# Kernel optimization log

Hardware: AMD Instinct MI355X
Metric: run time of the kernel (lower is better)

## Reference

```python
import jax, jax.numpy as jnp
import numpy as np

EPS = 1e-5
B, C, H, W, K = 16, 512, 64, 64, 32


def setup_inputs() -> dict:
    key = jax.random.key(0)
    ks = jax.random.split(key, 6)
    std = 1.0 / float(np.sqrt(K * C))
    return {
        "x": jax.random.normal(ks[0], (B, C, H, W), jnp.float32),
        "conv_w": jax.random.normal(ks[1], (C, C), jnp.float32) * (1.0 / np.sqrt(C)),
        "bn2_g": jnp.ones((C,), jnp.float32),
        "bn2_b": jnp.zeros((C,), jnp.float32),
        "bn2_m": jnp.zeros((C,), jnp.float32),
        "bn2_v": jnp.ones((C,), jnp.float32),
        "codewords": jax.random.uniform(ks[2], (K, C), jnp.float32, -std, std),
        "scale": jax.random.uniform(ks[3], (K,), jnp.float32, -1.0, 0.0),
        "bn1_g": jnp.ones((K,), jnp.float32),
        "bn1_b": jnp.zeros((K,), jnp.float32),
        "bn1_m": jnp.zeros((K,), jnp.float32),
        "bn1_v": jnp.ones((K,), jnp.float32),
        "fc_w": jax.random.normal(ks[4], (C, C), jnp.float32) * (1.0 / np.sqrt(C)),
        "fc_b": jnp.zeros((C,), jnp.float32),
    }


def reference(x, conv_w, bn2_g, bn2_b, bn2_m, bn2_v, codewords, scale,
              bn1_g, bn1_b, bn1_m, bn1_v, fc_w, fc_b):
    b, c, h, w = x.shape
    k = codewords.shape[0]
    # encoding_project: 1x1 conv (no bias) + BatchNorm2d (inference) + ReLU
    proj = jnp.einsum('oc,bchw->bohw', conv_w, x)
    s2 = (jax.lax.rsqrt(bn2_v + EPS) * bn2_g)[None, :, None, None]
    proj = jax.nn.relu((proj - bn2_m[None, :, None, None]) * s2 + bn2_b[None, :, None, None])
    # Encoding: scaled-L2 softmax assignment + residual aggregation
    feats = proj.reshape(b, c, h * w).transpose(0, 2, 1)          # (B, N, C)
    x2 = jnp.sum(feats * feats, axis=-1)                          # (B, N)
    c2 = jnp.sum(codewords * codewords, axis=-1)                  # (K,)
    xc = jnp.einsum('bnc,kc->bnk', feats, codewords)              # (B, N, K)
    dist = scale[None, None, :] * (x2[..., None] - 2.0 * xc + c2[None, None, :])
    assign = jax.nn.softmax(dist, axis=2)                         # (B, N, K)
    # sum_n w[b,n,k] * (x[b,n,c] - c[k,c])  without materializing (B,N,K,C)
    encoded = (jnp.einsum('bnk,bnc->bkc', assign, feats)
               - jnp.einsum('bnk,kc->bkc', assign, codewords))    # (B, K, C)
    # BatchNorm1d over num_codes (inference) + ReLU
    s1 = (jax.lax.rsqrt(bn1_v + EPS) * bn1_g)[None, :, None]
    encoded = jax.nn.relu((encoded - bn1_m[None, :, None]) * s1 + bn1_b[None, :, None])
    encoding_feat = jnp.mean(encoded, axis=1)                     # (B, C)
    # fc -> sigmoid gate, residual relu
    gamma = jax.nn.sigmoid(encoding_feat @ fc_w.T + fc_b)         # (B, C)
    output = jax.nn.relu(x + x * gamma[:, :, None, None])
    return (encoding_feat, output)
```

## Files before the change

kernel.cpp:

```cpp
#include <hip/hip_runtime.h>
#include <hip/hip_bf16.h>

#define BB   16
#define CC   512
#define HWN  4096
#define KK   32
#define EPSF 1e-5f

typedef short bf16x8 __attribute__((ext_vector_type(8)));
typedef float f32x4  __attribute__((ext_vector_type(4)));

#define MFMA16 __builtin_amdgcn_mfma_f32_16x16x32_bf16

#define GLD16(g, l) __builtin_amdgcn_global_load_lds(                          \
    (const __attribute__((address_space(1))) void*)(g),                        \
    (__attribute__((address_space(3))) void*)(l), 16, 0, 0)

#define EADDR(o, n) ((o) * 136 + (((((n) >> 3) ^ (((o) >> 3) & 15))) << 3) + ((n) & 7))

static __device__ __forceinline__ unsigned short f2b(float f) {
    unsigned u = __builtin_bit_cast(unsigned, f);
    unsigned r = (u + 0x7FFFu + ((u >> 16) & 1u)) >> 16;
    return (unsigned short)r;
}

__global__ __launch_bounds__(256) void k_prep(const float* __restrict__ W,
                                              const float* __restrict__ cw,
                                              const float* __restrict__ scale,
                                              const float* __restrict__ g1,
                                              const float* __restrict__ b1,
                                              const float* __restrict__ m1,
                                              const float* __restrict__ v1,
                                              unsigned short* __restrict__ Wb,
                                              unsigned short* __restrict__ cwb,
                                              float* __restrict__ sc2,
                                              float* __restrict__ s1,
                                              float* __restrict__ t1) {
    int bid = blockIdx.x, t = threadIdx.x;
    if (bid < 256) {
        int i = (bid * 256 + t) * 4;
        float4 v = *(const float4*)(W + i);
        uint2 p;
        p.x = (unsigned)f2b(v.x) | ((unsigned)f2b(v.y) << 16);
        p.y = (unsigned)f2b(v.z) | ((unsigned)f2b(v.w) << 16);
        *(uint2*)(Wb + i) = p;
    } else if (bid < 272) {
        int i = ((bid - 256) * 256 + t) * 4;
        float4 v = *(const float4*)(cw + i);
        uint2 p;
        p.x = (unsigned)f2b(v.x) | ((unsigned)f2b(v.y) << 16);
        p.y = (unsigned)f2b(v.z) | ((unsigned)f2b(v.w) << 16);
        *(uint2*)(cwb + i) = p;
    } else {
        int k = t >> 3, l8 = t & 7;
        const float* row = cw + k * CC + l8 * 64;
        float s = 0.f;
#pragma unroll
        for (int i = 0; i < 16; i++) {
            float4 c4 = *(const float4*)(row + i * 4);
            s += c4.x * c4.x + c4.y * c4.y + c4.z * c4.z + c4.w * c4.w;
        }
        s += __shfl_xor(s, 1); s += __shfl_xor(s, 2); s += __shfl_xor(s, 4);
        if (l8 == 0) sc2[k] = scale[k] * s;
        if (t < KK) {
            float sv = rsqrtf(v1[t] + EPSF) * g1[t];
            s1[t] = sv;
            t1[t] = b1[t] - m1[t] * sv;
        }
    }
}

__global__ __launch_bounds__(256) void k_transpose(const float* __restrict__ x,
                                                   unsigned short* __restrict__ xT) {
    __shared__ float tile[64][65];
    int bid = blockIdx.x;
    int b   = bid >> 9;
    int rem = bid & 511;
    int c0  = (rem >> 6) * 64;
    int n0  = (rem & 63) * 64;
    int t = threadIdx.x;
#pragma unroll
    for (int p = 0; p < 4; p++) {
        int s = p * 256 + t;
        int row = s >> 4, col = (s & 15) * 4;
        float4 v = *(const float4*)(x + (size_t)(b * CC + c0 + row) * HWN + n0 + col);
        tile[row][col]     = v.x;
        tile[row][col + 1] = v.y;
        tile[row][col + 2] = v.z;
        tile[row][col + 3] = v.w;
    }
    __syncthreads();
    int nr = t >> 2;
    int cg = (t & 3) * 16;
    unsigned u[8];
#pragma unroll
    for (int j = 0; j < 8; j++) {
        u[j] = (unsigned)f2b(tile[cg + 2 * j][nr]) |
               ((unsigned)f2b(tile[cg + 2 * j + 1][nr]) << 16);
    }
    unsigned short* dst = xT + (size_t)(b * HWN + n0 + nr) * CC + c0 + cg;
    uint4 a; a.x = u[0]; a.y = u[1]; a.z = u[2]; a.w = u[3];
    uint4 c; c.x = u[4]; c.y = u[5]; c.z = u[6]; c.w = u[7];
    *(uint4*)(dst)     = a;
    *(uint4*)(dst + 8) = c;
}

__global__ __launch_bounds__(256) void k_conv_gemm(const unsigned short* __restrict__ xT,
                                                   const unsigned short* __restrict__ Wb,
                                                   const float* __restrict__ g2,
                                                   const float* __restrict__ b2,
                                                   const float* __restrict__ m2,
                                                   const float* __restrict__ v2,
                                                   unsigned short* __restrict__ feats,
                                                   unsigned short* __restrict__ featsT,
                                                   float* __restrict__ x2) {
    __shared__ __align__(16) short lds[17408];
    int bid = blockIdx.x;
    bid = (bid & 7) * 256 + (bid >> 3);
    int b   = bid >> 7;
    int rem = bid & 127;
    int m0  = (rem >> 2) * 128;
    int o0  = (rem & 3) * 128;
    int t = threadIdx.x, lane = t & 63, wave = t >> 6;
    int mb = (wave >> 1) * 64, ob = (wave & 1) * 64;
    int col_l = lane & 15, quad = lane >> 4;

    f32x4 zero = {0.f, 0.f, 0.f, 0.f};
    f32x4 acc[4][4];
#pragma unroll
    for (int i = 0; i < 4; i++)
#pragma unroll
        for (int j = 0; j < 4; j++) acc[i][j] = zero;

    const unsigned short* Abase = xT + (size_t)(b * HWN + m0) * CC;
    const unsigned short* Bbase = Wb + (size_t)o0 * CC;

#define CSTAGE(pp, bb) do {                                                   \
    int c0_ = (pp) * 32;                                                      \
    _Pragma("unroll")                                                         \
    for (int p2 = 0; p2 < 2; p2++) {                                          \
        int sbase = p2 * 256 + wave * 64;                                     \
        int s = sbase + lane;                                                 \
        int row = s >> 2, part = (s & 3) * 8;                                 \
        GLD16(Abase + (size_t)row * CC + c0_ + part,                          \
              (char*)lds + (bb) * 8192 + sbase * 16);                         \
        GLD16(Bbase + (size_t)row * CC + c0_ + part,                          \
              (char*)lds + 16384 + (bb) * 8192 + sbase * 16);                 \
    } } while (0)

#define CCOMP(bb) do {                                                        \
    bf16x8 af[4], bfv[4];                                                     \
    _Pragma("unroll")                                                         \
    for (int im = 0; im < 4; im++)                                            \
        af[im] = *(const bf16x8*)(&lds[(bb) * 4096 + (mb + im * 16 + col_l) * 32 + quad * 8]); \
    _Pragma("unroll")                                                         \
    for (int in = 0; in < 4; in++)                                            \
        bfv[in] = *(const bf16x8*)(&lds[8192 + (bb) * 4096 + (ob + in * 16 + col_l) * 32 + quad * 8]); \
    _Pragma("unroll")                                                         \
    for (int im = 0; im < 4; im++)                                            \
        _Pragma("unroll")                                                     \
        for (int in = 0; in < 4; in++)                                        \
            acc[im][in] = MFMA16(af[im], bfv[in], acc[im][in], 0, 0, 0);      \
    } while (0)

    CSTAGE(0, 0);
    for (int p = 0; p < 15; p++) {
        CSTAGE(p + 1, (p + 1) & 1);
        asm volatile("s_waitcnt vmcnt(4)" ::: "memory");
        __builtin_amdgcn_s_barrier();
        asm volatile("" ::: "memory");
        CCOMP(p & 1);
        asm volatile("s_waitcnt lgkmcnt(0)" ::: "memory");
        __builtin_amdgcn_s_barrier();
    }
    asm volatile("s_waitcnt vmcnt(0)" ::: "memory");
    __builtin_amdgcn_s_barrier();
    asm volatile("" ::: "memory");
    CCOMP(1);
    __syncthreads();

    float scv[4], offv[4];
#pragma unroll
    for (int in = 0; in < 4; in++) {
        int o = o0 + ob + in * 16 + col_l;
        float sv = rsqrtf(v2[o] + EPSF) * g2[o];
        scv[in]  = sv;
        offv[in] = b2[o] - m2[o] * sv;
    }
#pragma unroll
    for (int im = 0; im < 4; im++) {
        int n_l = mb + im * 16 + quad * 4;
        float vv[4][4];
#pragma unroll
        for (int in = 0; in < 4; in++)
#pragma unroll
            for (int r = 0; r < 4; r++)
                vv[in][r] = fmaxf(acc[im][in][r] * scv[in] + offv[in], 0.f);
#pragma unroll
        for (int in = 0; in < 4; in++) {
            int o_l = ob + in * 16 + col_l;
            uint2 pk;
            pk.x = (unsigned)f2b(vv[in][0]) | ((unsigned)f2b(vv[in][1]) << 16);
            pk.y = (unsigned)f2b(vv[in][2]) | ((unsigned)f2b(vv[in][3]) << 16);
            *(uint2*)(&lds[EADDR(o_l, n_l)]) = pk;
        }
#pragma unroll
        for (int r = 0; r < 4; r++) {
            float ss = vv[0][r] * vv[0][r] + vv[1][r] * vv[1][r] +
                       vv[2][r] * vv[2][r] + vv[3][r] * vv[3][r];
            ss += __shfl_xor(ss, 1); ss += __shfl_xor(ss, 2);
            ss += __shfl_xor(ss, 4); ss += __shfl_xor(ss, 8);
            if (col_l == 0) atomicAdd(&x2[b * HWN + m0 + n_l + r], ss);
        }
    }
    __syncthreads();

#pragma unroll
    for (int rr = 0; rr < 8; rr++) {
        int o = rr * 16 + (t >> 4);
        int n16 = t & 15;
        uint4 v = *(const uint4*)(&lds[EADDR(o, n16 * 8)]);
        *(uint4*)(featsT + (size_t)(b * CC + o0 + o) * HWN + m0 + n16 * 8) = v;
    }
#pragma unroll
    for (int rr = 0; rr < 8; rr++) {
        int n = rr * 16 + (t >> 4);
        int o16 = t & 15;
        unsigned u[4];
#pragma unroll
        for (int jj = 0; jj < 4; jj++) {
            unsigned short a = lds[EADDR(o16 * 8 + 2 * jj,     n)];
            unsigned short bsh = lds[EADDR(o16 * 8 + 2 * jj + 1, n)];
            u[jj] = (unsigned)a | ((unsigned)bsh << 16);
        }
        uint4 pk; pk.x = u[0]; pk.y = u[1]; pk.z = u[2]; pk.w = u[3];
        *(uint4*)(feats + (size_t)(b * HWN + m0 + n) * CC + o0 + o16 * 8) = pk;
    }
}

__global__ __launch_bounds__(256) void k_assign(const unsigned short* __restrict__ feats,
                                                const unsigned short* __restrict__ cwb,
                                                const float* __restrict__ x2,
                                                const float* __restrict__ scale,
                                                const float* __restrict__ sc2,
                                                unsigned short* __restrict__ assignT,
                                                float* __restrict__ asum) {
    __shared__ __align__(16) short lds2[24832];
    __shared__ float sl[KK], cl[KK];
    int bid = blockIdx.x;
    int b = bid >> 5, n0 = (bid & 31) * 128;
    int t = threadIdx.x, lane = t & 63, wave = t >> 6;
    int col_l = lane & 15, quad = lane >> 4;

#pragma unroll
    for (int p = 0; p < 8; p++) {
        int s = p * 256 + t;
        int row = s >> 6, c8 = (s & 63) * 8;
        *(uint4*)(&lds2[row * 520 + c8]) = *(const uint4*)(cwb + row * 512 + c8);
    }
    if (t < KK) { sl[t] = scale[t]; cl[t] = sc2[t]; }

    f32x4 zero = {0.f, 0.f, 0.f, 0.f};
    f32x4 acc[2][2];
    acc[0][0] = zero; acc[0][1] = zero; acc[1][0] = zero; acc[1][1] = zero;

    const unsigned short* Fbase = feats + (size_t)(b * HWN + n0) * CC;

#define ASTAGE(ci_, bb) do {                                                  \
    int c0_ = (ci_) * 32;                                                     \
    _Pragma("unroll")                                                         \
    for (int p2 = 0; p2 < 2; p2++) {                                          \
        int sbase = p2 * 256 + wave * 64;                                     \
        int s = sbase + lane;                                                 \
        GLD16(Fbase + (size_t)(s >> 2) * CC + c0_ + (s & 3) * 8,              \
              (char*)lds2 + 33280 + (bb) * 8192 + sbase * 16);                \
    } } while (0)

#define ACOMP(ci_, bb) do {                                                   \
    int c0_ = (ci_) * 32;                                                     \
    bf16x8 af0 = *(const bf16x8*)(&lds2[(col_l) * 520 + c0_ + quad * 8]);     \
    bf16x8 af1 = *(const bf16x8*)(&lds2[(16 + col_l) * 520 + c0_ + quad * 8]);\
    _Pragma("unroll")                                                         \
    for (int ct = 0; ct < 2; ct++) {                                          \
        bf16x8 bf = *(const bf16x8*)(&lds2[16640 + (bb) * 4096 +              \
                     (wave * 32 + ct * 16 + col_l) * 32 + quad * 8]);         \
        acc[0][ct] = MFMA16(af0, bf, acc[0][ct], 0, 0, 0);                    \
        acc[1][ct] = MFMA16(af1, bf, acc[1][ct], 0, 0, 0);                    \
    } } while (0)

    ASTAGE(0, 0);
    asm volatile("s_waitcnt lgkmcnt(0)" ::: "memory");
    for (int ci = 0; ci < 15; ci++) {
        ASTAGE(ci + 1, (ci + 1) & 1);
        asm volatile("s_waitcnt vmcnt(2)" ::: "memory");
        __builtin_amdgcn_s_barrier();
        asm volatile("" ::: "memory");
        ACOMP(ci, ci & 1);
        asm volatile("s_waitcnt lgkmcnt(0)" ::: "memory");
        __builtin_amdgcn_s_barrier();
    }
    asm volatile("s_waitcnt vmcnt(0)" ::: "memory");
    __builtin_amdgcn_s_barrier();
    asm volatile("" ::: "memory");
    ACOMP(15, 1);

    float asw[2][4];
#pragma unroll
    for (int mk = 0; mk < 2; mk++)
#pragma unroll
        for (int r = 0; r < 4; r++) asw[mk][r] = 0.f;

#pragma unroll
    for (int ct = 0; ct < 2; ct++) {
        int n = n0 + wave * 32 + ct * 16 + col_l;
        float x2v = x2[b * HWN + n];
        float d[2][4];
        float mmax = -3.4e38f;
#pragma unroll
        for (int mk = 0; mk < 2; mk++)
#pragma unroll
            for (int r = 0; r < 4; r++) {
                int k = mk * 16 + quad * 4 + r;
                d[mk][r] = sl[k] * (x2v - 2.f * acc[mk][ct][r]) + cl[k];
                mmax = fmaxf(mmax, d[mk][r]);
            }
        mmax = fmaxf(mmax, __shfl_xor(mmax, 16));
        mmax = fmaxf(mmax, __shfl_xor(mmax, 32));
        float ssum = 0.f;
#pragma unroll
        for (int mk = 0; mk < 2; mk++)
#pragma unroll
            for (int r = 0; r < 4; r++) {
                d[mk][r] = __expf(d[mk][r] - mmax);
                ssum += d[mk][r];
            }
        ssum += __shfl_xor(ssum, 16);
        ssum += __shfl_xor(ssum, 32);
        float rinv = 1.f / ssum;
#pragma unroll
        for (int mk = 0; mk < 2; mk++)
#pragma unroll
            for (int r = 0; r < 4; r++) {
                int k = mk * 16 + quad * 4 + r;
                float a = d[mk][r] * rinv;
                assignT[(size_t)(b * KK + k) * HWN + n] = f2b(a);
                float p = a;
                p += __shfl_xor(p, 1); p += __shfl_xor(p, 2);
                p += __shfl_xor(p, 4); p += __shfl_xor(p, 8);
                asw[mk][r] += p;
            }
    }
#pragma unroll
    for (int mk = 0; mk < 2; mk++)
#pragma unroll
        for (int r = 0; r < 4; r++)
            if (col_l == 0)
                atomicAdd(&asum[b * KK + mk * 16 + quad * 4 + r], asw[mk][r]);
}

__global__ __launch_bounds__(256) void k_encode(const unsigned short* __restrict__ featsT,
                                                const unsigned short* __restrict__ assignT,
                                                float* __restrict__ enc) {
    __shared__ __align__(16) short lds3[20480];
    int bid = blockIdx.x;
    int b   = bid >> 5;
    int rem = bid & 31;
    int c0  = (rem >> 3) * 128;
    int ns  = rem & 7;
    int t = threadIdx.x, lane = t & 63, wave = t >> 6;
    int col_l = lane & 15, quad = lane >> 4;

    f32x4 zero = {0.f, 0.f, 0.f, 0.f};
    f32x4 acc[2][2];
    acc[0][0] = zero; acc[0][1] = zero; acc[1][0] = zero; acc[1][1] = zero;

    const unsigned short* Abase = featsT + (size_t)(b * CC + c0) * HWN;
    const unsigned short* Bbase = assignT + (size_t)(b * KK) * HWN;

#define ESTAGE(it_, bb) do {                                                  \
    int n0_ = ns * 512 + (it_) * 64;                                          \
    _Pragma("unroll")                                                         \
    for (int pc = 0; pc < 2; pc++)                                            \
        _Pragma("unroll")                                                     \
        for (int p2 = 0; p2 < 2; p2++) {                                      \
            int sbase = p2 * 256 + wave * 64;                                 \
            int s = sbase + lane;                                             \
            GLD16(Abase + (size_t)(s >> 2) * HWN + n0_ + pc * 32 + (s & 3) * 8, \
                  (char*)lds3 + (bb) * 16384 + pc * 8192 + sbase * 16);       \
        }                                                                     \
    {   int s = t;                                                            \
        int pan = s >> 7, row = (s & 127) >> 2, part = (s & 3) * 8;           \
        GLD16(Bbase + (size_t)row * HWN + n0_ + pan * 32 + part,              \
              (char*)lds3 + 32768 + (bb) * 4096 +                             \
              ((wave >> 1) * 2048 + (wave & 1) * 1024) + lane * 16);          \
    } } while (0)

#define ECOMP(bb) do {                                                        \
    _Pragma("unroll")                                                         \
    for (int pc = 0; pc < 2; pc++) {                                          \
        bf16x8 a0 = *(const bf16x8*)(&lds3[(bb) * 8192 + pc * 4096 + (wave * 32 + col_l) * 32 + quad * 8]); \
        bf16x8 a1 = *(const bf16x8*)(&lds3[(bb) * 8192 + pc * 4096 + (wave * 32 + 16 + col_l) * 32 + quad * 8]); \
        bf16x8 b0 = *(const bf16x8*)(&lds3[16384 + (bb) * 2048 + pc * 1024 + (col_l) * 32 + quad * 8]); \
        bf16x8 b1 = *(const bf16x8*)(&lds3[16384 + (bb) * 2048 + pc * 1024 + (16 + col_l) * 32 + quad * 8]); \
        acc[0][0] = MFMA16(a0, b0, acc[0][0], 0, 0, 0);                       \
        acc[0][1] = MFMA16(a0, b1, acc[0][1], 0, 0, 0);                       \
        acc[1][0] = MFMA16(a1, b0, acc[1][0], 0, 0, 0);                       \
        acc[1][1] = MFMA16(a1, b1, acc[1][1], 0, 0, 0);                       \
    } } while (0)

    ESTAGE(0, 0);
    for (int it = 0; it < 7; it++) {
        ESTAGE(it + 1, (it + 1) & 1);
        asm volatile("s_waitcnt vmcnt(5)" ::: "memory");
        __builtin_amdgcn_s_barrier();
        asm volatile("" ::: "memory");
        ECOMP(it & 1);
        asm volatile("s_waitcnt lgkmcnt(0)" ::: "memory");
        __builtin_amdgcn_s_barrier();
    }
    asm volatile("s_waitcnt vmcnt(0)" ::: "memory");
    __builtin_amdgcn_s_barrier();
    asm volatile("" ::: "memory");
    ECOMP(1);

#pragma unroll
    for (int i2 = 0; i2 < 2; i2++)
#pragma unroll
        for (int ck = 0; ck < 2; ck++)
#pragma unroll
            for (int r = 0; r < 4; r++) {
                int c = c0 + wave * 32 + i2 * 16 + quad * 4 + r;
                int k = ck * 16 + col_l;
                atomicAdd(&enc[(size_t)(b * CC + c) * KK + k], acc[i2][ck][r]);
            }
}

__global__ __launch_bounds__(256) void k_efeat(const float* __restrict__ enc,
                                               const float* __restrict__ asum,
                                               const float* __restrict__ cwf,
                                               const float* __restrict__ s1,
                                               const float* __restrict__ t1,
                                               float* __restrict__ efeat) {
    __shared__ float asl[KK], s1l[KK], t1l[KK];
    int b = blockIdx.x, t = threadIdx.x;
    if (t < KK) { asl[t] = asum[b * KK + t]; s1l[t] = s1[t]; t1l[t] = t1[t]; }
    __syncthreads();
#pragma unroll
    for (int cc = 0; cc < 2; cc++) {
        int c = cc * 256 + t;
        const float* er = enc + (size_t)(b * CC + c) * KK;
        float s = 0.f;
#pragma unroll
        for (int k = 0; k < KK; k++) {
            float v = (er[k] - asl[k] * cwf[k * CC + c]) * s1l[k] + t1l[k];
            s += fmaxf(v, 0.f);
        }
        efeat[b * CC + c] = s * (1.f / 32.f);
    }
}

__global__ __launch_bounds__(256) void k_fc(const float* __restrict__ efeat,
                                            const float* __restrict__ fcw,
                                            const float* __restrict__ fcb,
                                            float* __restrict__ gamma) {
    __shared__ float ef[CC];
    int bid = blockIdx.x;
    int b  = bid >> 1;
    int o0 = (bid & 1) * 256;
    int t = threadIdx.x;
    if (t < 128) *(float4*)(&ef[t * 4]) = *(const float4*)(efeat + b * CC + t * 4);
    __syncthreads();
    int o = o0 + t;
    float a = fcb[o];
    const float* wrow = fcw + (size_t)o * CC;
#pragma unroll 4
    for (int c4 = 0; c4 < 128; c4++) {
        float4 w = *(const float4*)(wrow + c4 * 4);
        float4 e = *(const float4*)(&ef[c4 * 4]);
        a += w.x * e.x + w.y * e.y + w.z * e.z + w.w * e.w;
    }
    gamma[b * CC + o] = 1.f / (1.f + __expf(-a));
}

__global__ __launch_bounds__(256) void k_gate(const float* __restrict__ x,
                                              const float* __restrict__ gamma,
                                              float* __restrict__ out) {
    int bid = blockIdx.x;
    float g = 1.f + gamma[bid];
    const float* xr = x + ((size_t)bid << 12);
    float* orow = out + ((size_t)bid << 12);
    int t4 = threadIdx.x * 4;
#pragma unroll
    for (int u = 0; u < 4; u++) {
        float4 v = *(const float4*)(xr + u * 1024 + t4);
        v.x = fmaxf(v.x * g, 0.f);
        v.y = fmaxf(v.y * g, 0.f);
        v.z = fmaxf(v.z * g, 0.f);
        v.w = fmaxf(v.w * g, 0.f);
        *(float4*)(orow + u * 1024 + t4) = v;
    }
}

extern "C" void kernel_launch(void* const* d_in, const int* in_sizes, int n_in,
                              void* d_out, int out_size, void* d_ws, size_t ws_size,
                              hipStream_t stream) {
    const float* x      = (const float*)d_in[0];
    const float* conv_w = (const float*)d_in[1];
    const float* bn2_g  = (const float*)d_in[2];
    const float* bn2_b  = (const float*)d_in[3];
    const float* bn2_m  = (const float*)d_in[4];
    const float* bn2_v  = (const float*)d_in[5];
    const float* cw     = (const float*)d_in[6];
    const float* scale  = (const float*)d_in[7];
    const float* bn1_g  = (const float*)d_in[8];
    const float* bn1_b  = (const float*)d_in[9];
    const float* bn1_m  = (const float*)d_in[10];
    const float* bn1_v  = (const float*)d_in[11];
    const float* fc_w   = (const float*)d_in[12];
    const float* fc_b   = (const float*)d_in[13];

    float* outf = (float*)d_out;
    char* ws = (char*)d_ws;

    unsigned short* feats   = (unsigned short*)(ws);
    unsigned short* assignT = (unsigned short*)(ws + 67108864);
    unsigned short* Wb      = (unsigned short*)(ws + 71303168);
    unsigned short* cwb     = (unsigned short*)(ws + 71827456);
    float*          x2      = (float*)(ws + 71860224);
    float*          asum    = (float*)(ws + 72122368);
    float*          enc     = (float*)(ws + 72124416);
    float*          sc2     = (float*)(ws + 73172992);
    float*          s1      = (float*)(ws + 73173248);
    float*          t1      = (float*)(ws + 73173504);
    float*          gamma   = (float*)(ws + 73173760);

    unsigned short* xT     = (unsigned short*)((char*)d_out + 32768);
    unsigned short* featsT = (unsigned short*)((char*)d_out + 67141632);

    hipMemsetAsync(x2, 0, 262144 + 2048 + 1048576, stream);

    k_prep<<<273, 256, 0, stream>>>(conv_w, cw, scale, bn1_g, bn1_b, bn1_m, bn1_v,
                                    Wb, cwb, sc2, s1, t1);
    k_transpose<<<8192, 256, 0, stream>>>(x, xT);
    k_conv_gemm<<<2048, 256, 0, stream>>>(xT, Wb, bn2_g, bn2_b, bn2_m, bn2_v,
                                          feats, featsT, x2);
    k_assign<<<512, 256, 0, stream>>>(feats, cwb, x2, scale, sc2, assignT, asum);
    k_encode<<<512, 256, 0, stream>>>(featsT, assignT, enc);
    k_efeat<<<16, 256, 0, stream>>>(enc, asum, cw, s1, t1, outf);
    k_fc<<<32, 256, 0, stream>>>(outf, fc_w, fc_b, gamma);
    k_gate<<<8192, 256, 0, stream>>>(x, gamma, outf + 8192);
}
```

Measured before the change: 433.6 us.

## Fuse fp32-to-bf16 transpose into conv GEMM A-tile loading

Removes the separate transpose kernel. The conv GEMM now reads fp32 x directly into registers, converts it to bf16 with packed cvt instructions and writes a swizzled transposed A tile into LDS. The B operand moves to a triple-buffered async pipeline with register prefetch of A two stages ahead, and launch bounds request 4 blocks per CU. This saves a full write and reread of the bf16 transposed activation through HBM, at the cost of more VGPR pressure and scalar LDS stores inside the GEMM main loop.

Measured after the change: 420.5 us. 3.0% less time.

```diff
diff --git a/kernel.cpp b/kernel.cpp
--- a/kernel.cpp
+++ b/kernel.cpp
@@ -70,51 +70,18 @@
     }
 }
 
-__global__ __launch_bounds__(256) void k_transpose(const float* __restrict__ x,
-                                                   unsigned short* __restrict__ xT) {
-    __shared__ float tile[64][65];
-    int bid = blockIdx.x;
-    int b   = bid >> 9;
-    int rem = bid & 511;
-    int c0  = (rem >> 6) * 64;
-    int n0  = (rem & 63) * 64;
-    int t = threadIdx.x;
-#pragma unroll
-    for (int p = 0; p < 4; p++) {
-        int s = p * 256 + t;
-        int row = s >> 4, col = (s & 15) * 4;
-        float4 v = *(const float4*)(x + (size_t)(b * CC + c0 + row) * HWN + n0 + col);
-        tile[row][col]     = v.x;
-        tile[row][col + 1] = v.y;
-        tile[row][col + 2] = v.z;
-        tile[row][col + 3] = v.w;
-    }
-    __syncthreads();
-    int nr = t >> 2;
-    int cg = (t & 3) * 16;
-    unsigned u[8];
-#pragma unroll
-    for (int j = 0; j < 8; j++) {
-        u[j] = (unsigned)f2b(tile[cg + 2 * j][nr]) |
-               ((unsigned)f2b(tile[cg + 2 * j + 1][nr]) << 16);
-    }
-    unsigned short* dst = xT + (size_t)(b * HWN + n0 + nr) * CC + c0 + cg;
-    uint4 a; a.x = u[0]; a.y = u[1]; a.z = u[2]; a.w = u[3];
-    uint4 c; c.x = u[4]; c.y = u[5]; c.z = u[6]; c.w = u[7];
-    *(uint4*)(dst)     = a;
-    *(uint4*)(dst + 8) = c;
-}
-
-__global__ __launch_bounds__(256) void k_conv_gemm(const unsigned short* __restrict__ xT,
-                                                   const unsigned short* __restrict__ Wb,
-                                                   const float* __restrict__ g2,
-                                                   const float* __restrict__ b2,
-                                                   const float* __restrict__ m2,
-                                                   const float* __restrict__ v2,
-                                                   unsigned short* __restrict__ feats,
-                                                   unsigned short* __restrict__ featsT,
-                                                   float* __restrict__ x2) {
-    __shared__ __align__(16) short lds[17408];
+#define AADDR(n, c) ((n) * 32 + (((((c) >> 3) ^ (((n) >> 3) & 3)) & 3) << 3) + ((c) & 7))
+
+__global__ __launch_bounds__(256, 4) void k_conv_gemm(const float* __restrict__ x,
+                                                      const unsigned short* __restrict__ Wb,
+                                                      const float* __restrict__ g2,
+                                                      const float* __restrict__ b2,
+                                                      const float* __restrict__ m2,
+                                                      const float* __restrict__ v2,
+                                                      unsigned short* __restrict__ feats,
+                                                      unsigned short* __restrict__ featsT,
+                                                      float* __restrict__ x2) {
+    __shared__ __align__(16) short lds[20480];
     int bid = blockIdx.x;
     bid = (bid & 7) * 256 + (bid >> 3);
     int b   = bid >> 7;
@@ -124,6 +91,8 @@
     int t = threadIdx.x, lane = t & 63, wave = t >> 6;
     int mb = (wave >> 1) * 64, ob = (wave & 1) * 64;
     int col_l = lane & 15, quad = lane >> 4;
+    int pc = t >> 4;
+    int ch = t & 15;
 
     f32x4 zero = {0.f, 0.f, 0.f, 0.f};
     f32x4 acc[4][4];
@@ -132,30 +101,60 @@
 #pragma unroll
         for (int j = 0; j < 4; j++) acc[i][j] = zero;
 
-    const unsigned short* Abase = xT + (size_t)(b * HWN + m0) * CC;
+    const float* Xp = x + (size_t)(b * CC) * HWN + m0 + ch * 8;
     const unsigned short* Bbase = Wb + (size_t)o0 * CC;
 
-#define CSTAGE(pp, bb) do {                                                   \
+    float4 a0, a1, a2, a3;
+
+#define CLOAD_A(pp) do {                                                      \
+    const float* r0_ = Xp + (size_t)((pp) * 32 + 2 * pc) * HWN;               \
+    a0 = *(const float4*)(r0_);       a1 = *(const float4*)(r0_ + 4);         \
+    a2 = *(const float4*)(r0_ + HWN); a3 = *(const float4*)(r0_ + HWN + 4);   \
+} while (0)
+
+#define CLOAD_B(pp, bb3) do {                                                 \
     int c0_ = (pp) * 32;                                                      \
     _Pragma("unroll")                                                         \
     for (int p2 = 0; p2 < 2; p2++) {                                          \
         int sbase = p2 * 256 + wave * 64;                                     \
         int s = sbase + lane;                                                 \
-        int row = s >> 2, part = (s & 3) * 8;                                 \
-        GLD16(Abase + (size_t)row * CC + c0_ + part,                          \
-              (char*)lds + (bb) * 8192 + sbase * 16);                         \
-        GLD16(Bbase + (size_t)row * CC + c0_ + part,                          \
-              (char*)lds + 16384 + (bb) * 8192 + sbase * 16);                 \
+        GLD16(Bbase + (size_t)(s >> 2) * CC + c0_ + (s & 3) * 8,              \
+              (char*)lds + 16384 + (bb3) * 8192 + sbase * 16);                \
     } } while (0)
 
-#define CCOMP(bb) do {                                                        \
+#define CWRITE_A(ab) do {                                                     \
+    unsigned q0, q1, q2, q3, q4, q5, q6, q7;                                  \
+    asm("v_cvt_pk_bf16_f32 %0, %1, %2" : "=v"(q0) : "v"(a0.x), "v"(a2.x));    \
+    asm("v_cvt_pk_bf16_f32 %0, %1, %2" : "=v"(q1) : "v"(a0.y), "v"(a2.y));    \
+    asm("v_cvt_pk_bf16_f32 %0, %1, %2" : "=v"(q2) : "v"(a0.z), "v"(a2.z));    \
+    asm("v_cvt_pk_bf16_f32 %0, %1, %2" : "=v"(q3) : "v"(a0.w), "v"(a2.w));    \
+    asm("v_cvt_pk_bf16_f32 %0, %1, %2" : "=v"(q4) : "v"(a1.x), "v"(a3.x));    \
+    asm("v_cvt_pk_bf16_f32 %0, %1, %2" : "=v"(q5) : "v"(a1.y), "v"(a3.y));    \
+    asm("v_cvt_pk_bf16_f32 %0, %1, %2" : "=v"(q6) : "v"(a1.z), "v"(a3.z));    \
+    asm("v_cvt_pk_bf16_f32 %0, %1, %2" : "=v"(q7) : "v"(a1.w), "v"(a3.w));    \
+    int base_ = (ab) * 4096 + ch * 256 +                                      \
+                ((((pc >> 2) ^ (ch & 3)) & 3) << 3) + ((2 * pc) & 7);         \
+    *(unsigned*)(&lds[base_ +   0]) = q0;                                     \
+    *(unsigned*)(&lds[base_ +  32]) = q1;                                     \
+    *(unsigned*)(&lds[base_ +  64]) = q2;                                     \
+    *(unsigned*)(&lds[base_ +  96]) = q3;                                     \
+    *(unsigned*)(&lds[base_ + 128]) = q4;                                     \
+    *(unsigned*)(&lds[base_ + 160]) = q5;                                     \
+    *(unsigned*)(&lds[base_ + 192]) = q6;                                     \
+    *(unsigned*)(&lds[base_ + 224]) = q7;                                     \
+} while (0)
+
+#define CCOMP(ab, bb3) do {                                                   \
     bf16x8 af[4], bfv[4];                                                     \
     _Pragma("unroll")                                                         \
-    for (int im = 0; im < 4; im++)                                            \
-        af[im] = *(const bf16x8*)(&lds[(bb) * 4096 + (mb + im * 16 + col_l) * 32 + quad * 8]); \
+    for (int im = 0; im < 4; im++) {                                          \
+        int nl = mb + im * 16 + col_l;                                        \
+        af[im] = *(const bf16x8*)(&lds[(ab) * 4096 + AADDR(nl, quad * 8)]);   \
+    }                                                                         \
     _Pragma("unroll")                                                         \
     for (int in = 0; in < 4; in++)                                            \
-        bfv[in] = *(const bf16x8*)(&lds[8192 + (bb) * 4096 + (ob + in * 16 + col_l) * 32 + quad * 8]); \
+        bfv[in] = *(const bf16x8*)(&lds[8192 + (bb3) * 4096 +                 \
+                   (ob + in * 16 + col_l) * 32 + quad * 8]);                  \
     _Pragma("unroll")                                                         \
     for (int im = 0; im < 4; im++)                                            \
         _Pragma("unroll")                                                     \
@@ -163,20 +162,33 @@
             acc[im][in] = MFMA16(af[im], bfv[in], acc[im][in], 0, 0, 0);      \
     } while (0)
 
-    CSTAGE(0, 0);
-    for (int p = 0; p < 15; p++) {
-        CSTAGE(p + 1, (p + 1) & 1);
-        asm volatile("s_waitcnt vmcnt(4)" ::: "memory");
+    CLOAD_A(0); CLOAD_B(0, 0);
+    CWRITE_A(0);
+    CLOAD_A(1); CLOAD_B(1, 1);
+    asm volatile("s_waitcnt lgkmcnt(0)" ::: "memory");
+    asm volatile("s_waitcnt vmcnt(6)" ::: "memory");
+    __builtin_amdgcn_s_barrier();
+    asm volatile("" ::: "memory");
+
+    int bi = 0;
+    for (int p = 0; p < 14; ++p) {
+        CCOMP(p & 1, bi);
+        CWRITE_A((p + 1) & 1);
+        int bi2 = bi >= 1 ? bi - 1 : 2;
+        CLOAD_A(p + 2); CLOAD_B(p + 2, bi2);
+        asm volatile("s_waitcnt lgkmcnt(0)" ::: "memory");
+        asm volatile("s_waitcnt vmcnt(6)" ::: "memory");
         __builtin_amdgcn_s_barrier();
         asm volatile("" ::: "memory");
-        CCOMP(p & 1);
-        asm volatile("s_waitcnt lgkmcnt(0)" ::: "memory");
-        __builtin_amdgcn_s_barrier();
-    }
+        bi = bi == 2 ? 0 : bi + 1;
+    }
+    CCOMP(0, 2);
+    CWRITE_A(1);
+    asm volatile("s_waitcnt lgkmcnt(0)" ::: "memory");
     asm volatile("s_waitcnt vmcnt(0)" ::: "memory");
     __builtin_amdgcn_s_barrier();
     asm volatile("" ::: "memory");
-    CCOMP(1);
+    CCOMP(1, 0);
     __syncthreads();
 
     float scv[4], offv[4];
@@ -380,13 +392,13 @@
 #define ESTAGE(it_, bb) do {                                                  \
     int n0_ = ns * 512 + (it_) * 64;                                          \
     _Pragma("unroll")                                                         \
-    for (int pc = 0; pc < 2; pc++)                                            \
+    for (int pc_ = 0; pc_ < 2; pc_++)                                         \
         _Pragma("unroll")                                                     \
         for (int p2 = 0; p2 < 2; p2++) {                                      \
             int sbase = p2 * 256 + wave * 64;                                 \
             int s = sbase + lane;                                             \
-            GLD16(Abase + (size_t)(s >> 2) * HWN + n0_ + pc * 32 + (s & 3) * 8, \
-                  (char*)lds3 + (bb) * 16384 + pc * 8192 + sbase * 16);       \
+            GLD16(Abase + (size_t)(s >> 2) * HWN + n0_ + pc_ * 32 + (s & 3) * 8, \
+                  (char*)lds3 + (bb) * 16384 + pc_ * 8192 + sbase * 16);      \
         }                                                                     \
     {   int s = t;                                                            \
         int pan = s >> 7, row = (s & 127) >> 2, part = (s & 3) * 8;           \
@@ -397,11 +409,11 @@
 
 #define ECOMP(bb) do {                                                        \
     _Pragma("unroll")                                                         \
-    for (int pc = 0; pc < 2; pc++) {                                          \
-        bf16x8 a0 = *(const bf16x8*)(&lds3[(bb) * 8192 + pc * 4096 + (wave * 32 + col_l) * 32 + quad * 8]); \
-        bf16x8 a1 = *(const bf16x8*)(&lds3[(bb) * 8192 + pc * 4096 + (wave * 32 + 16 + col_l) * 32 + quad * 8]); \
-        bf16x8 b0 = *(const bf16x8*)(&lds3[16384 + (bb) * 2048 + pc * 1024 + (col_l) * 32 + quad * 8]); \
-        bf16x8 b1 = *(const bf16x8*)(&lds3[16384 + (bb) * 2048 + pc * 1024 + (16 + col_l) * 32 + quad * 8]); \
+    for (int pc_ = 0; pc_ < 2; pc_++) {                                       \
+        bf16x8 a0 = *(const bf16x8*)(&lds3[(bb) * 8192 + pc_ * 4096 + (wave * 32 + col_l) * 32 + quad * 8]); \
+        bf16x8 a1 = *(const bf16x8*)(&lds3[(bb) * 8192 + pc_ * 4096 + (wave * 32 + 16 + col_l) * 32 + quad * 8]); \
+        bf16x8 b0 = *(const bf16x8*)(&lds3[16384 + (bb) * 2048 + pc_ * 1024 + (col_l) * 32 + quad * 8]); \
+        bf16x8 b1 = *(const bf16x8*)(&lds3[16384 + (bb) * 2048 + pc_ * 1024 + (16 + col_l) * 32 + quad * 8]); \
         acc[0][0] = MFMA16(a0, b0, acc[0][0], 0, 0, 0);                       \
         acc[0][1] = MFMA16(a0, b1, acc[0][1], 0, 0, 0);                       \
         acc[1][0] = MFMA16(a1, b0, acc[1][0], 0, 0, 0);                       \
@@ -534,15 +546,13 @@
     float*          t1      = (float*)(ws + 73173504);
     float*          gamma   = (float*)(ws + 73173760);
 
-    unsigned short* xT     = (unsigned short*)((char*)d_out + 32768);
     unsigned short* featsT = (unsigned short*)((char*)d_out + 67141632);
 
     hipMemsetAsync(x2, 0, 262144 + 2048 + 1048576, stream);
 
     k_prep<<<273, 256, 0, stream>>>(conv_w, cw, scale, bn1_g, bn1_b, bn1_m, bn1_v,
                                     Wb, cwb, sc2, s1, t1);
-    k_transpose<<<8192, 256, 0, stream>>>(x, xT);
-    k_conv_gemm<<<2048, 256, 0, stream>>>(xT, Wb, bn2_g, bn2_b, bn2_m, bn2_v,
+    k_conv_gemm<<<2048, 256, 0, stream>>>(x, Wb, bn2_g, bn2_b, bn2_m, bn2_v,
                                           feats, featsT, x2);
     k_assign<<<512, 256, 0, stream>>>(feats, cwb, x2, scale, sc2, assignT, asum);
     k_encode<<<512, 256, 0, stream>>>(featsT, assignT, enc);
```
